# Optimization experiments

Hardware: AMD Instinct MI355X
Metric: run time of the kernel (lower is better)

The kernel has to match this reference:

```python
import jax, jax.numpy as jnp
import numpy as np

LMAX, MMAX = 6, 2
CIN = COUT = 128
NUM_EDGES = 50000
NUM_M_COMP = (LMAX + 1) + sum(2 * (LMAX + 1 - m) for m in range(1, MMAX + 1))  # 29


def setup_inputs() -> dict:
    key = jax.random.key(0)
    ks = jax.random.split(key, 4)
    x = jax.random.normal(ks[0], (NUM_EDGES, NUM_M_COMP, CIN), dtype=jnp.float32)
    d0 = (LMAX + 1) * CIN  # 896
    W0 = jax.random.normal(ks[1], (d0, d0), dtype=jnp.float32) / np.float32(np.sqrt(d0))
    b0 = jnp.zeros((d0,), dtype=jnp.float32)
    Ws = []
    for i, m in enumerate(range(1, MMAX + 1)):
        din = (LMAX + 1 - m) * CIN
        dout = (LMAX + 1 - m) * COUT
        # torch Linear init then mul_(1/sqrt(2)); random scaled init suffices for a baseline
        Ws.append(jax.random.normal(ks[2 + i], (2 * dout, din), dtype=jnp.float32)
                  / np.float32(np.sqrt(2.0) * np.sqrt(din)))
    return {"x": x, "W0": W0, "b0": b0, "W1": Ws[0], "W2": Ws[1]}


def reference(x, W0, b0, W1, W2):
    E = x.shape[0]
    Wm = [W1, W2]
    outs = []
    # m = 0 block: flatten (lmax+1, Cin) -> single Linear with bias
    x0 = x[:, :LMAX + 1].reshape(E, (LMAX + 1) * CIN)
    y0 = x0 @ W0.T + b0                               # [E, (lmax+1)*Cout]
    outs.append(y0.reshape(E, LMAX + 1, COUT))
    offset = LMAX + 1
    for m in range(1, MMAX + 1):
        n = LMAX + 1 - m
        xm = x[:, offset:offset + 2 * n].reshape(E, 2, n * CIN)  # [E, 2(real/imag), n*Cin]
        offset += 2 * n
        ym = jnp.einsum('eti,oi->eto', xm, Wm[m - 1])            # [E, 2, 2*n*Cout]
        of = n * COUT
        x_r, x_i = ym[..., :of], ym[..., of:]
        pos = x_r[:, 0] - x_i[:, 1]                              # [E, n*Cout]
        neg = x_r[:, 1] + x_i[:, 0]
        outs.append(pos.reshape(E, n, COUT))
        outs.append(neg.reshape(E, n, COUT))
    return jnp.concatenate(outs, axis=1)  # [E, num_m_components, Cout]
```

## Files before the change

kernel.cpp:

```cpp
#include <hip/hip_runtime.h>
#include <hip/hip_bf16.h>
#include <cstdint>
#include <cstddef>

typedef __bf16 bf16_t;
typedef __bf16 bf16x8 __attribute__((ext_vector_type(8)));
typedef __bf16 bf16x4 __attribute__((ext_vector_type(4)));
typedef float f32x4 __attribute__((ext_vector_type(4)));

static constexpr int LD = 29 * 128;

template <int N> struct IC { static constexpr int v = N; };


__global__ void cvt_w0_pad_kernel(const float* __restrict__ in, bf16_t* __restrict__ out,
                                  int rows_real, int kdim, int total) {
    int idx = blockIdx.x * 256 + threadIdx.x;
    if (idx >= total) return;
    int r = idx / kdim;
    int c = idx - r * kdim;
    out[idx] = (bf16_t)((r < rows_real) ? in[(size_t)r * kdim + c] : 0.f);
}

__global__ void combine_wm_kernel(const float* __restrict__ W, bf16_t* __restrict__ Wc,
                                  int of, int din, int total) {
    int idx = blockIdx.x * 256 + threadIdx.x;
    if (idx >= total) return;
    int twodin = 2 * din;
    int r = idx / twodin;
    int c = idx - r * twodin;
    float v;
    if (r < of) {
        v = (c < din) ? W[(size_t)r * din + c]
                      : -W[(size_t)(r + of) * din + (c - din)];
    } else {
        int j = r - of;
        v = (c < din) ? W[(size_t)(j + of) * din + c]
                      : W[(size_t)j * din + (c - din)];
    }
    Wc[idx] = (bf16_t)v;
}

__global__ void cvt_x_kernel(const float* __restrict__ in, bf16_t* __restrict__ out, long n8) {
    long stride = (long)gridDim.x * 256;
    for (long i = blockIdx.x * 256L + threadIdx.x; i < n8; i += stride) {
        f32x4 v0 = *(const f32x4*)(in + i * 8);
        f32x4 v1 = *(const f32x4*)(in + i * 8 + 4);
        bf16x8 h;
        h[0] = (bf16_t)v0[0]; h[1] = (bf16_t)v0[1];
        h[2] = (bf16_t)v0[2]; h[3] = (bf16_t)v0[3];
        h[4] = (bf16_t)v1[0]; h[5] = (bf16_t)v1[1];
        h[6] = (bf16_t)v1[2]; h[7] = (bf16_t)v1[3];
        *(bf16x8*)(out + i * 8) = h;
    }
}


#define MMA_Q(QM, QN, AF)                                                            \
    do {                                                                             \
        __builtin_amdgcn_s_setprio(1);                                               \
        _Pragma("unroll") for (int i_ = 0; i_ < 2; ++i_)                             \
        _Pragma("unroll") for (int j_ = 0; j_ < 4; ++j_)                             \
        _Pragma("unroll") for (int kk_ = 0; kk_ < 2; ++kk_)                          \
            acc[QM][QN][i_][j_] = __builtin_amdgcn_mfma_f32_16x16x32_bf16(           \
                AF[i_][kk_], b[j_][kk_], acc[QM][QN][i_][j_], 0, 0, 0);              \
        __builtin_amdgcn_s_setprio(0);                                               \
    } while (0)

#define BAR() __builtin_amdgcn_s_barrier()
#define LGKM0()                                                   \
    do {                                                          \
        asm volatile("s_waitcnt lgkmcnt(0)" ::: "memory");        \
        __builtin_amdgcn_sched_barrier(0);                        \
    } while (0)

typedef bf16_t lds_t[2][2][2][128][64];

template <int K, int NT, bool BIAS>
__device__ __forceinline__ void gemm_tile_body(
        const bf16_t* __restrict__ A,
        const bf16_t* __restrict__ Wn,
        const float* __restrict__ biasn,
        float* __restrict__ Yn,
        long m0, int ncol, int E, lds_t& lds) {
    constexpr int NIT = NT / 2;
    static_assert(NT % 2 == 0, "NT even");

    const int tid  = threadIdx.x;
    const int wid  = tid >> 6;
    const int lane = tid & 63;
    const int awr  = wid & 3;
    const int bwc  = wid >> 2;
    const int lrow = lane & 15;
    const int koff = lane >> 4;
    const int sr   = tid >> 3;
    const int sc   = tid & 7;

    int offA[2][2], offB[4][2];
    #pragma unroll
    for (int i = 0; i < 2; ++i)
        #pragma unroll
        for (int kk = 0; kk < 2; ++kk) {
            const int rr = awr * 32 + i * 16 + lrow;
            offA[i][kk] = rr * 128 + (((kk * 4 + koff) ^ (rr & 7)) * 16);
        }
    #pragma unroll
    for (int j = 0; j < 4; ++j)
        #pragma unroll
        for (int kk = 0; kk < 2; ++kk) {
            const int rr = bwc * 64 + j * 16 + lrow;
            offB[j][kk] = rr * 128 + (((kk * 4 + koff) ^ (rr & 7)) * 16);
        }

    const bf16_t* gA[2][2];
    const bf16_t* gB[2][2];
    #pragma unroll
    for (int hf = 0; hf < 2; ++hf)
        #pragma unroll
        for (int s = 0; s < 2; ++s) {
            const int r  = s * 64 + sr;
            const int kc = sc ^ (r & 7);
            long grow = m0 + hf * 128 + r;
            if (grow >= E) grow = E - 1;
            gA[hf][s] = A + grow * (long)LD + kc * 8;
            gB[hf][s] = Wn + (size_t)(hf * 128 + r) * K + kc * 8;
        }
    const int dstw = wid * 1024;

    bf16x8 a0[2][2], a1[2][2], b[4][2];
    f32x4 acc[2][2][2][4] = {};

    auto stage = [&](auto BUc, auto OPc, auto HFc, int kt) {
        constexpr int BU = decltype(BUc)::v;
        constexpr int OP = decltype(OPc)::v;
        constexpr int HF = decltype(HFc)::v;
        const long kof = (long)kt * 64;
        #pragma unroll
        for (int s = 0; s < 2; ++s) {
            const bf16_t* gsrc = (OP ? gB[HF][s] : gA[HF][s]) + kof;
            char* dst = (char*)&lds[BU][OP][HF][0][0] + s * 8192 + dstw;
            __builtin_amdgcn_global_load_lds(
                (const __attribute__((address_space(1))) void*)gsrc,
                (__attribute__((address_space(3))) void*)dst, 16, 0, 0);
        }
    };

    auto load_a = [&](bf16x8 (&a)[2][2], auto BUc, auto HFc) {
        constexpr int BU = decltype(BUc)::v;
        constexpr int HF = decltype(HFc)::v;
        const char* base = (const char*)&lds[BU][0][HF][0][0];
        #pragma unroll
        for (int i = 0; i < 2; ++i)
            #pragma unroll
            for (int kk = 0; kk < 2; ++kk)
                a[i][kk] = *(const bf16x8*)(base + offA[i][kk]);
    };
    auto load_b = [&](auto BUc, auto HFc) {
        constexpr int BU = decltype(BUc)::v;
        constexpr int HF = decltype(HFc)::v;
        const char* base = (const char*)&lds[BU][1][HF][0][0];
        #pragma unroll
        for (int j = 0; j < 4; ++j)
            #pragma unroll
            for (int kk = 0; kk < 2; ++kk)
                b[j][kk] = *(const bf16x8*)(base + offB[j][kk]);
    };

    auto half_iter = [&](auto BUc, auto STc, int skt) {
        constexpr int ST = decltype(STc)::v;
        load_a(a0, BUc, IC<0>{});
        load_b(BUc, IC<0>{});
        BAR(); LGKM0();
        MMA_Q(0, 0, a0);
        BAR();
        load_a(a1, BUc, IC<1>{});
        if constexpr (ST) { stage(BUc, IC<0>{}, IC<0>{}, skt); stage(BUc, IC<1>{}, IC<0>{}, skt); }
        BAR(); LGKM0();
        MMA_Q(1, 0, a1);
        BAR();
        load_b(BUc, IC<1>{});
        if constexpr (ST) stage(BUc, IC<0>{}, IC<1>{}, skt);
        BAR(); LGKM0();
        MMA_Q(1, 1, a1);
        BAR();
        if constexpr (ST) {
            stage(BUc, IC<1>{}, IC<1>{}, skt);
            asm volatile("s_waitcnt vmcnt(8)" ::: "memory");
        } else {
            asm volatile("s_waitcnt vmcnt(0)" ::: "memory");
        }
        BAR(); LGKM0();
        MMA_Q(0, 1, a0);
        BAR();
    };

    stage(IC<0>{}, IC<0>{}, IC<0>{}, 0); stage(IC<0>{}, IC<0>{}, IC<1>{}, 0);
    stage(IC<0>{}, IC<1>{}, IC<0>{}, 0); stage(IC<0>{}, IC<1>{}, IC<1>{}, 0);
    stage(IC<1>{}, IC<0>{}, IC<0>{}, 1); stage(IC<1>{}, IC<0>{}, IC<1>{}, 1);
    stage(IC<1>{}, IC<1>{}, IC<0>{}, 1); stage(IC<1>{}, IC<1>{}, IC<1>{}, 1);
    asm volatile("s_waitcnt vmcnt(8)" ::: "memory");
    BAR();

    #pragma unroll 1
    for (int it = 0; it < NIT - 1; ++it) {
        half_iter(IC<0>{}, IC<1>{}, 2 * it + 2);
        half_iter(IC<1>{}, IC<1>{}, 2 * it + 3);
    }
    half_iter(IC<0>{}, IC<0>{}, 0);
    half_iter(IC<1>{}, IC<0>{}, 0);

    #pragma unroll
    for (int qm = 0; qm < 2; ++qm)
        #pragma unroll
        for (int qn = 0; qn < 2; ++qn)
            #pragma unroll
            for (int j = 0; j < 4; ++j) {
                const int col = qn * 128 + bwc * 64 + j * 16 + lrow;
                if (col < ncol) {
                    float bv = 0.f;
                    if constexpr (BIAS) bv = biasn[col];
                    #pragma unroll
                    for (int i = 0; i < 2; ++i) {
                        const long rb = m0 + qm * 128 + awr * 32 + i * 16 + koff * 4;
                        #pragma unroll
                        for (int r = 0; r < 4; ++r) {
                            const long row = rb + r;
                            if (row < E) Yn[row * LD + col] = acc[qm][qn][i][j][r] + bv;
                        }
                    }
                }
            }
}

__device__ __forceinline__ int seg_remap(int lb, int ncol, int mt) {
    const int g8   = (mt >> 3) << 3;
    const int full = g8 * ncol;
    if (lb < full) {
        const int x  = lb & 7;
        const int s  = lb >> 3;
        const int s4 = s / ncol;
        const int mem = s - s4 * ncol;
        return (s4 * 8 + x) * ncol + mem;
    }
    return lb;
}

__global__ __launch_bounds__(512, 2)
void gemm_all_kernel(const bf16_t* __restrict__ xb,
                     const bf16_t* __restrict__ w0,
                     const bf16_t* __restrict__ w1,
                     const bf16_t* __restrict__ w2,
                     const float* __restrict__ b0,
                     float* __restrict__ out,
                     int E, int mt) {
    __shared__ lds_t lds;

    const int b  = blockIdx.x;
    const int S0 = 4 * mt;
    const int S1 = S0 + 6 * mt;

    if (b < S0) {
        const int lt = seg_remap(b, 4, mt);
        const int mi = lt >> 2, ni = lt & 3;
        const int ncol = (ni == 3) ? 128 : 256;
        gemm_tile_body<896, 14, true>(xb, w0 + (size_t)ni * 256 * 896, b0 + ni * 256,
                                      out + ni * 256, (long)mi * 256, ncol, E, lds);
    } else if (b < S1) {
        const int lt = seg_remap(b - S0, 6, mt);
        const int mi = lt / 6, ni = lt - mi * 6;
        gemm_tile_body<1536, 24, false>(xb + 896, w1 + (size_t)ni * 256 * 1536, nullptr,
                                        out + 896 + ni * 256, (long)mi * 256, 256, E, lds);
    } else {
        const int lt = seg_remap(b - S1, 5, mt);
        const int mi = lt / 5, ni = lt - mi * 5;
        gemm_tile_body<1280, 20, false>(xb + 2432, w2 + (size_t)ni * 256 * 1280, nullptr,
                                        out + 2432 + ni * 256, (long)mi * 256, 256, E, lds);
    }
}


template <int N, int K, bool BIAS>
__global__ __launch_bounds__(256)
void gemm_fb_kernel(const float* __restrict__ X, const bf16_t* __restrict__ W,
                    const float* __restrict__ bias, float* __restrict__ Y, int M) {
    constexpr int BM = 128, BK = 32;
    constexpr int KT = K / BK;
    __shared__ bf16_t As[BM][BK + 8];
    __shared__ bf16_t Bs[BM][BK];
    const int tid = threadIdx.x, wid = tid >> 6, lane = tid & 63;
    const int wr = wid >> 1, wc = wid & 1;
    const int m0 = blockIdx.y * BM, n0 = blockIdx.x * 128;
    const int srow0 = wid * 16 + (lane >> 2), schunk = lane & 3;
    const int ar = tid >> 3, ac = (tid & 7) * 4;
    const int lrow = lane & 15, koff = lane >> 4;
    f32x4 acc[4][4] = {};
    for (int kt = 0; kt < KT; ++kt) {
        const int k0 = kt * BK;
        #pragma unroll
        for (int s = 0; s < 2; ++s) {
            const int row = srow0 + s * 64;
            const int kc = schunk ^ ((row >> 1) & 3);
            const bf16_t* gsrc = W + (size_t)(n0 + row) * K + k0 + kc * 8;
            bf16_t* ldsbase = &Bs[wid * 16 + s * 64][0];
            __builtin_amdgcn_global_load_lds(
                (const __attribute__((address_space(1))) void*)gsrc,
                (__attribute__((address_space(3))) void*)ldsbase, 16, 0, 0);
        }
        #pragma unroll
        for (int p = 0; p < 4; ++p) {
            const int row = p * 32 + ar;
            const int gr = m0 + row;
            f32x4 v = {};
            if (gr < M) v = *(const f32x4*)(X + (size_t)gr * LD + k0 + ac);
            bf16x4 h;
            h[0] = (bf16_t)v[0]; h[1] = (bf16_t)v[1];
            h[2] = (bf16_t)v[2]; h[3] = (bf16_t)v[3];
            *(bf16x4*)(&As[row][ac]) = h;
        }
        __syncthreads();
        bf16x8 a[4], bb[4];
        #pragma unroll
        for (int i = 0; i < 4; ++i) {
            a[i] = *(const bf16x8*)(&As[wr * 64 + i * 16 + lrow][koff * 8]);
            const int col = wc * 64 + i * 16 + lrow;
            const int kc = koff ^ ((col >> 1) & 3);
            bb[i] = *(const bf16x8*)(&Bs[col][kc * 8]);
        }
        #pragma unroll
        for (int i = 0; i < 4; ++i)
            #pragma unroll
            for (int j = 0; j < 4; ++j)
                acc[i][j] = __builtin_amdgcn_mfma_f32_16x16x32_bf16(a[i], bb[j], acc[i][j], 0, 0, 0);
        __syncthreads();
    }
    #pragma unroll
    for (int j = 0; j < 4; ++j) {
        const int col = n0 + wc * 64 + j * 16 + lrow;
        float bv = 0.f;
        if constexpr (BIAS) bv = bias[col];
        #pragma unroll
        for (int i = 0; i < 4; ++i) {
            const int rbase = m0 + wr * 64 + i * 16 + koff * 4;
            #pragma unroll
            for (int r = 0; r < 4; ++r) {
                const int gr = rbase + r;
                if (gr < M) Y[(size_t)gr * LD + col] = acc[i][j][r] + bv;
            }
        }
    }
}


extern "C" void kernel_launch(void* const* d_in, const int* in_sizes, int n_in,
                              void* d_out, int out_size, void* d_ws, size_t ws_size,
                              hipStream_t stream) {
    const float* x  = (const float*)d_in[0];
    const float* W0 = (const float*)d_in[1];
    const float* b0 = (const float*)d_in[2];
    const float* W1 = (const float*)d_in[3];
    const float* W2 = (const float*)d_in[4];
    float* out = (float*)d_out;

    const int E = in_sizes[0] / LD;

    constexpr size_t W0P = (size_t)1024 * 896;
    constexpr size_t W1S = (size_t)1536 * 1536;
    constexpr size_t W2S = (size_t)1280 * 1280;
    bf16_t* wc0 = (bf16_t*)d_ws;
    bf16_t* wc1 = wc0 + W0P;
    bf16_t* wc2 = wc1 + W1S;
    bf16_t* xb  = wc2 + W2S;

    const size_t need = (W0P + W1S + W2S + (size_t)E * LD) * sizeof(bf16_t);
    const bool fast = ws_size >= need;

    cvt_w0_pad_kernel<<<(int)((W0P + 255) / 256), 256, 0, stream>>>(W0, wc0, 896, 896, (int)W0P);
    combine_wm_kernel<<<(int)(W1S / 256), 256, 0, stream>>>(W1, wc1, 768, 768, (int)W1S);
    combine_wm_kernel<<<(int)(W2S / 256), 256, 0, stream>>>(W2, wc2, 640, 640, (int)W2S);

    if (fast) {
        const long n8 = (long)E * LD / 8;
        cvt_x_kernel<<<4096, 256, 0, stream>>>(x, xb, n8);
        const int mt = (E + 255) / 256;
        gemm_all_kernel<<<dim3(15 * mt), 512, 0, stream>>>(xb, wc0, wc1, wc2, b0, out, E, mt);
    } else {
        const int mt = (E + 127) / 128;
        gemm_fb_kernel<896, 896, true>
            <<<dim3(896 / 128, mt), 256, 0, stream>>>(x, wc0, b0, out, E);
        gemm_fb_kernel<1536, 1536, false>
            <<<dim3(1536 / 128, mt), 256, 0, stream>>>(x + 896, wc1, nullptr, out + 896, E);
        gemm_fb_kernel<1280, 1280, false>
            <<<dim3(1280 / 128, mt), 256, 0, stream>>>(x + 2432, wc2, nullptr, out + 2432, E);
    }
}
```

Baseline: 797.0 us.

## Prefetch next buffer's A/B fragments from LDS during final MMA quadrant

Restructures the GEMM main loop to double-buffer register fragments. The next k-tile's A0 and B half-0 fragments are loaded from LDS while the current tile's last MMA quadrant runs, and B is split into two register sets. Full lgkmcnt(0) waits become partial waits so LDS reads overlap with MFMA work. In exchange, register pressure rises from the extra fragment buffers, and the partial wait counts must exactly match the order in which loads are issued.

```diff
diff --git a/kernel.cpp b/kernel.cpp
--- a/kernel.cpp
+++ b/kernel.cpp
@@ -11,6 +11,8 @@
 static constexpr int LD = 29 * 128;
 
 template <int N> struct IC { static constexpr int v = N; };
+template <int S, typename T>
+__device__ __forceinline__ T& sel(T& x, T& y) { if constexpr (S == 0) return x; else return y; }
 
 
 __global__ void cvt_w0_pad_kernel(const float* __restrict__ in, bf16_t* __restrict__ out,
@@ -56,22 +58,23 @@
 }
 
 
-#define MMA_Q(QM, QN, AF)                                                            \
+#define MMA_Q(QM, QN, AF, BF)                                                        \
     do {                                                                             \
         __builtin_amdgcn_s_setprio(1);                                               \
         _Pragma("unroll") for (int i_ = 0; i_ < 2; ++i_)                             \
         _Pragma("unroll") for (int j_ = 0; j_ < 4; ++j_)                             \
         _Pragma("unroll") for (int kk_ = 0; kk_ < 2; ++kk_)                          \
             acc[QM][QN][i_][j_] = __builtin_amdgcn_mfma_f32_16x16x32_bf16(           \
-                AF[i_][kk_], b[j_][kk_], acc[QM][QN][i_][j_], 0, 0, 0);              \
+                AF[i_][kk_], BF[j_][kk_], acc[QM][QN][i_][j_], 0, 0, 0);             \
         __builtin_amdgcn_s_setprio(0);                                               \
     } while (0)
 
 #define BAR() __builtin_amdgcn_s_barrier()
-#define LGKM0()                                                   \
-    do {                                                          \
-        asm volatile("s_waitcnt lgkmcnt(0)" ::: "memory");        \
-        __builtin_amdgcn_sched_barrier(0);                        \
+#define VMC(N) asm volatile("s_waitcnt vmcnt(" #N ")" ::: "memory")
+#define LGK(N)                                                           \
+    do {                                                                 \
+        asm volatile("s_waitcnt lgkmcnt(" #N ")" ::: "memory");          \
+        __builtin_amdgcn_sched_barrier(0);                               \
     } while (0)
 
 typedef bf16_t lds_t[2][2][2][128][64];
@@ -127,7 +130,7 @@
         }
     const int dstw = wid * 1024;
 
-    bf16x8 a0[2][2], a1[2][2], b[4][2];
+    bf16x8 a0A[2][2], a0B[2][2], a1[2][2], bH0[4][2], bH1[4][2];
     f32x4 acc[2][2][2][4] = {};
 
     auto stage = [&](auto BUc, auto OPc, auto HFc, int kt) {
@@ -155,7 +158,7 @@
             for (int kk = 0; kk < 2; ++kk)
                 a[i][kk] = *(const bf16x8*)(base + offA[i][kk]);
     };
-    auto load_b = [&](auto BUc, auto HFc) {
+    auto load_b = [&](bf16x8 (&bb)[4][2], auto BUc, auto HFc) {
         constexpr int BU = decltype(BUc)::v;
         constexpr int HF = decltype(HFc)::v;
         const char* base = (const char*)&lds[BU][1][HF][0][0];
@@ -163,34 +166,46 @@
         for (int j = 0; j < 4; ++j)
             #pragma unroll
             for (int kk = 0; kk < 2; ++kk)
-                b[j][kk] = *(const bf16x8*)(base + offB[j][kk]);
+                bb[j][kk] = *(const bf16x8*)(base + offB[j][kk]);
     };
 
-    auto half_iter = [&](auto BUc, auto STc, int skt) {
+    auto half_iter = [&](auto BUc, auto ASc, auto STc, auto HNc, int skt) {
+        constexpr int BU = decltype(BUc)::v;
+        constexpr int AS = decltype(ASc)::v;
         constexpr int ST = decltype(STc)::v;
-        load_a(a0, BUc, IC<0>{});
-        load_b(BUc, IC<0>{});
-        BAR(); LGKM0();
-        MMA_Q(0, 0, a0);
+        constexpr int HN = decltype(HNc)::v;
+        bf16x8 (&a0u)[2][2] = sel<AS>(a0A, a0B);
+        bf16x8 (&a0n)[2][2] = sel<AS ^ 1>(a0A, a0B);
+
+        load_a(a1, BUc, IC<1>{});
+        BAR(); LGK(4);
+        MMA_Q(0, 0, a0u, bH0);
         BAR();
-        load_a(a1, BUc, IC<1>{});
+        load_b(bH1, BUc, IC<1>{});
         if constexpr (ST) { stage(BUc, IC<0>{}, IC<0>{}, skt); stage(BUc, IC<1>{}, IC<0>{}, skt); }
-        BAR(); LGKM0();
-        MMA_Q(1, 0, a1);
+        BAR(); LGK(8);
+        MMA_Q(1, 0, a1, bH0);
         BAR();
-        load_b(BUc, IC<1>{});
         if constexpr (ST) stage(BUc, IC<0>{}, IC<1>{}, skt);
-        BAR(); LGKM0();
-        MMA_Q(1, 1, a1);
+        BAR(); LGK(0);
+        MMA_Q(1, 1, a1, bH1);
         BAR();
         if constexpr (ST) {
             stage(BUc, IC<1>{}, IC<1>{}, skt);
-            asm volatile("s_waitcnt vmcnt(8)" ::: "memory");
+            VMC(8);
         } else {
-            asm volatile("s_waitcnt vmcnt(0)" ::: "memory");
-        }
-        BAR(); LGKM0();
-        MMA_Q(0, 1, a0);
+            VMC(0);
+        }
+        BAR();
+        if constexpr (HN) {
+            __builtin_amdgcn_sched_barrier(0);
+            load_a(a0n, IC<BU ^ 1>{}, IC<0>{});
+            load_b(bH0, IC<BU ^ 1>{}, IC<0>{});
+            LGK(12);
+        } else {
+            LGK(0);
+        }
+        MMA_Q(0, 1, a0u, bH1);
         BAR();
     };
 
@@ -198,16 +213,19 @@
     stage(IC<0>{}, IC<1>{}, IC<0>{}, 0); stage(IC<0>{}, IC<1>{}, IC<1>{}, 0);
     stage(IC<1>{}, IC<0>{}, IC<0>{}, 1); stage(IC<1>{}, IC<0>{}, IC<1>{}, 1);
     stage(IC<1>{}, IC<1>{}, IC<0>{}, 1); stage(IC<1>{}, IC<1>{}, IC<1>{}, 1);
-    asm volatile("s_waitcnt vmcnt(8)" ::: "memory");
+    VMC(8);
     BAR();
+    __builtin_amdgcn_sched_barrier(0);
+    load_a(a0A, IC<0>{}, IC<0>{});
+    load_b(bH0, IC<0>{}, IC<0>{});
 
     #pragma unroll 1
     for (int it = 0; it < NIT - 1; ++it) {
-        half_iter(IC<0>{}, IC<1>{}, 2 * it + 2);
-        half_iter(IC<1>{}, IC<1>{}, 2 * it + 3);
-    }
-    half_iter(IC<0>{}, IC<0>{}, 0);
-    half_iter(IC<1>{}, IC<0>{}, 0);
+        half_iter(IC<0>{}, IC<0>{}, IC<1>{}, IC<1>{}, 2 * it + 2);
+        half_iter(IC<1>{}, IC<1>{}, IC<1>{}, IC<1>{}, 2 * it + 3);
+    }
+    half_iter(IC<0>{}, IC<0>{}, IC<0>{}, IC<1>{}, 0);
+    half_iter(IC<1>{}, IC<1>{}, IC<0>{}, IC<0>{}, 0);
 
     #pragma unroll
     for (int qm = 0; qm < 2; ++qm)
```

Result: slower. 1.102 ms (+38.3%).

## Restructure GEMM main loop to one barrier per k-tile with full-tile prefetch

Applied to the files above, without the earlier changes.

Replaces the four-phase half-iteration schedule, which used many barriers and staggered partial staging, with a simpler double-buffered loop. Each k-tile now prefetches the whole next tile into the other LDS buffer, loads all A fragments plus B in two halves, runs all four MMA quadrants, then waits for vmcnt(0) and takes a single barrier. The aim is to cut barrier and synchronisation overhead per k-step. In exchange the prefetch distance drops to one tile and more A fragments stay live in registers, which may expose global-load latency and raise register pressure.

```diff
diff --git a/kernel.cpp b/kernel.cpp
--- a/kernel.cpp
+++ b/kernel.cpp
@@ -63,15 +63,16 @@
         _Pragma("unroll") for (int j_ = 0; j_ < 4; ++j_)                             \
         _Pragma("unroll") for (int kk_ = 0; kk_ < 2; ++kk_)                          \
             acc[QM][QN][i_][j_] = __builtin_amdgcn_mfma_f32_16x16x32_bf16(           \
-                AF[i_][kk_], b[j_][kk_], acc[QM][QN][i_][j_], 0, 0, 0);              \
+                AF[i_][kk_], bb[j_][kk_], acc[QM][QN][i_][j_], 0, 0, 0);             \
         __builtin_amdgcn_s_setprio(0);                                               \
     } while (0)
 
 #define BAR() __builtin_amdgcn_s_barrier()
-#define LGKM0()                                                   \
-    do {                                                          \
-        asm volatile("s_waitcnt lgkmcnt(0)" ::: "memory");        \
-        __builtin_amdgcn_sched_barrier(0);                        \
+#define VMC(N) asm volatile("s_waitcnt vmcnt(" #N ")" ::: "memory")
+#define LGK(N)                                                           \
+    do {                                                                 \
+        asm volatile("s_waitcnt lgkmcnt(" #N ")" ::: "memory");          \
+        __builtin_amdgcn_sched_barrier(0);                               \
     } while (0)
 
 typedef bf16_t lds_t[2][2][2][128][64];
@@ -127,7 +128,7 @@
         }
     const int dstw = wid * 1024;
 
-    bf16x8 a0[2][2], a1[2][2], b[4][2];
+    bf16x8 aH0[2][2], aH1[2][2], bb[4][2];
     f32x4 acc[2][2][2][4] = {};
 
     auto stage = [&](auto BUc, auto OPc, auto HFc, int kt) {
@@ -144,6 +145,10 @@
                 (__attribute__((address_space(3))) void*)dst, 16, 0, 0);
         }
     };
+    auto stage_tile = [&](auto BUc, int kt) {
+        stage(BUc, IC<0>{}, IC<0>{}, kt); stage(BUc, IC<0>{}, IC<1>{}, kt);
+        stage(BUc, IC<1>{}, IC<0>{}, kt); stage(BUc, IC<1>{}, IC<1>{}, kt);
+    };
 
     auto load_a = [&](bf16x8 (&a)[2][2], auto BUc, auto HFc) {
         constexpr int BU = decltype(BUc)::v;
@@ -163,51 +168,37 @@
         for (int j = 0; j < 4; ++j)
             #pragma unroll
             for (int kk = 0; kk < 2; ++kk)
-                b[j][kk] = *(const bf16x8*)(base + offB[j][kk]);
-    };
-
-    auto half_iter = [&](auto BUc, auto STc, int skt) {
-        constexpr int ST = decltype(STc)::v;
-        load_a(a0, BUc, IC<0>{});
+                bb[j][kk] = *(const bf16x8*)(base + offB[j][kk]);
+    };
+
+    auto kt_body = [&](auto BUc, auto STc, int skt) {
+        constexpr int BU = decltype(BUc)::v;
+        if constexpr (decltype(STc)::v) stage_tile(IC<BU ^ 1>{}, skt);
+        load_a(aH0, BUc, IC<0>{});
+        load_a(aH1, BUc, IC<1>{});
         load_b(BUc, IC<0>{});
-        BAR(); LGKM0();
-        MMA_Q(0, 0, a0);
+        LGK(0);
+        MMA_Q(0, 0, aH0);
+        MMA_Q(1, 0, aH1);
+        load_b(BUc, IC<1>{});
+        LGK(0);
+        MMA_Q(1, 1, aH1);
+        MMA_Q(0, 1, aH0);
+        VMC(0);
         BAR();
-        load_a(a1, BUc, IC<1>{});
-        if constexpr (ST) { stage(BUc, IC<0>{}, IC<0>{}, skt); stage(BUc, IC<1>{}, IC<0>{}, skt); }
-        BAR(); LGKM0();
-        MMA_Q(1, 0, a1);
-        BAR();
-        load_b(BUc, IC<1>{});
-        if constexpr (ST) stage(BUc, IC<0>{}, IC<1>{}, skt);
-        BAR(); LGKM0();
-        MMA_Q(1, 1, a1);
-        BAR();
-        if constexpr (ST) {
-            stage(BUc, IC<1>{}, IC<1>{}, skt);
-            asm volatile("s_waitcnt vmcnt(8)" ::: "memory");
-        } else {
-            asm volatile("s_waitcnt vmcnt(0)" ::: "memory");
-        }
-        BAR(); LGKM0();
-        MMA_Q(0, 1, a0);
-        BAR();
-    };
-
-    stage(IC<0>{}, IC<0>{}, IC<0>{}, 0); stage(IC<0>{}, IC<0>{}, IC<1>{}, 0);
-    stage(IC<0>{}, IC<1>{}, IC<0>{}, 0); stage(IC<0>{}, IC<1>{}, IC<1>{}, 0);
-    stage(IC<1>{}, IC<0>{}, IC<0>{}, 1); stage(IC<1>{}, IC<0>{}, IC<1>{}, 1);
-    stage(IC<1>{}, IC<1>{}, IC<0>{}, 1); stage(IC<1>{}, IC<1>{}, IC<1>{}, 1);
-    asm volatile("s_waitcnt vmcnt(8)" ::: "memory");
+    };
+
+    stage_tile(IC<0>{}, 0);
+    VMC(0);
     BAR();
 
     #pragma unroll 1
     for (int it = 0; it < NIT - 1; ++it) {
-        half_iter(IC<0>{}, IC<1>{}, 2 * it + 2);
-        half_iter(IC<1>{}, IC<1>{}, 2 * it + 3);
-    }
-    half_iter(IC<0>{}, IC<0>{}, 0);
-    half_iter(IC<1>{}, IC<0>{}, 0);
+        kt_body(IC<0>{}, IC<1>{}, 2 * it + 1);
+        kt_body(IC<1>{}, IC<1>{}, 2 * it + 2);
+    }
+    kt_body(IC<0>{}, IC<1>{}, NT - 1);
+    kt_body(IC<1>{}, IC<0>{}, 0);
 
     #pragma unroll
     for (int qm = 0; qm < 2; ++qm)
@@ -318,19 +309,19 @@
             *(bf16x4*)(&As[row][ac]) = h;
         }
         __syncthreads();
-        bf16x8 a[4], bb[4];
+        bf16x8 a[4], bbf[4];
         #pragma unroll
         for (int i = 0; i < 4; ++i) {
             a[i] = *(const bf16x8*)(&As[wr * 64 + i * 16 + lrow][koff * 8]);
             const int col = wc * 64 + i * 16 + lrow;
             const int kc = koff ^ ((col >> 1) & 3);
-            bb[i] = *(const bf16x8*)(&Bs[col][kc * 8]);
+            bbf[i] = *(const bf16x8*)(&Bs[col][kc * 8]);
         }
         #pragma unroll
         for (int i = 0; i < 4; ++i)
             #pragma unroll
             for (int j = 0; j < 4; ++j)
-                acc[i][j] = __builtin_amdgcn_mfma_f32_16x16x32_bf16(a[i], bb[j], acc[i][j], 0, 0, 0);
+                acc[i][j] = __builtin_amdgcn_mfma_f32_16x16x32_bf16(a[i], bbf[j], acc[i][j], 0, 0, 0);
         __syncthreads();
     }
     #pragma unroll
```

Result: no change. 802.1 us, median of 2 (+0.6%).
